# Kernel tuning notes

Measured on AMD Instinct MI355X. Metric: run time of the kernel, lower is better.

## Reference

```python
import jax, jax.numpy as jnp
import numpy as np

N_NEURON = 1024
N_PEPTIDE = 16
N_GENES = 1
BATCH = 2048
SQ = 32  # int(sqrt(N_NEURON))
DT = 1.0 / 120.0
STATE_SIZE = N_NEURON + N_GENES + N_NEURON + N_NEURON * N_PEPTIDE  # 18433


def setup_inputs() -> dict:
    key = jax.random.key(0)
    ks = jax.random.split(key, 10)
    # structured state: [ablate_mat | pc2 | neuron | peptide]
    ablate_mat = jnp.ones((BATCH, N_NEURON), jnp.float32)
    pc2 = jax.random.uniform(ks[0], (BATCH, N_GENES), jnp.float32)
    neuron = jax.random.normal(ks[1], (BATCH, N_NEURON), jnp.float32)
    peptide = jax.random.uniform(ks[2], (BATCH, N_NEURON * N_PEPTIDE), jnp.float32)
    state = jnp.concatenate([ablate_mat, pc2, neuron, peptide], axis=-1)
    u = jax.random.normal(ks[3], (BATCH, 1), jnp.float32)
    # uniform noise sample used by the exp firing noise; keep strictly < 1
    noise_u = jax.random.uniform(ks[4], (BATCH, N_NEURON), jnp.float32, 1e-6, 1.0 - 1e-6)
    D = jax.random.uniform(ks[5], (N_PEPTIDE,), jnp.float32)
    pep_prod_rate = jax.random.uniform(ks[6], (N_PEPTIDE,), jnp.float32)
    pep_decay_rate = jax.random.uniform(ks[7], (N_PEPTIDE,), jnp.float32)
    pep_action = jax.random.normal(ks[8], (N_PEPTIDE,), jnp.float32)
    synapse_matrix = jax.random.normal(ks[9], (N_NEURON, N_NEURON), jnp.float32) * 0.02
    neuron_decay = jnp.ones((1,), jnp.float32) * 0.5
    input_layer = jax.random.normal(jax.random.fold_in(key, 11), (N_NEURON,), jnp.float32)
    return dict(u=u, state=state, noise_u=noise_u, D=D, pep_prod_rate=pep_prod_rate,
                pep_decay_rate=pep_decay_rate, pep_action=pep_action,
                synapse_matrix=synapse_matrix, neuron_decay=neuron_decay,
                input_layer=input_layer)


def reference(u, state, noise_u, D, pep_prod_rate, pep_decay_rate, pep_action,
              synapse_matrix, neuron_decay, input_layer):
    # func = abs (log_train=False)
    Dp = jnp.abs(D)
    prod_r = jnp.abs(pep_prod_rate)
    decay_r = jnp.abs(pep_decay_rate)
    ndecay = jnp.abs(neuron_decay)

    # unpack state: [ablate | pc2 | neuron | peptide]
    ablate_mat = state[:, :N_NEURON]
    pc2 = state[:, N_NEURON:N_NEURON + N_GENES]
    neuron = state[:, N_NEURON + N_GENES:2 * N_NEURON + N_GENES]
    pep_flat = state[:, 2 * N_NEURON + N_GENES:]
    peptide = pep_flat.reshape(-1, N_NEURON, N_PEPTIDE)

    firing = jax.nn.relu(neuron) * ablate_mat
    neuron = neuron * ablate_mat

    # noisy_fire, noise='exp': firing = -(firing+0.01)*log(1-U)
    firing = -(firing + 0.01) * jnp.log1p(-noise_u)
    firing = jnp.clip(firing, 0.0, 10.0)

    # peptide production / decay
    pep_prod = prod_r * firing[:, :, None]           # (b, n, p)
    pep_decay = decay_r * peptide                    # (b, n, p)

    # wrap-around 2D Laplacian diffusion stencil on (SQ, SQ) grid
    ps = peptide.reshape(-1, SQ, SQ, N_PEPTIDE)
    lap = (jnp.roll(ps, -1, axis=1) + jnp.roll(ps, 1, axis=1)
           + jnp.roll(ps, -1, axis=2) + jnp.roll(ps, 1, axis=2) - 4.0 * ps)
    pep_diffuse = (Dp * lap).reshape(-1, N_NEURON, N_PEPTIDE)

    # neuron dynamics
    d_neuron = jnp.sum(peptide * pep_action, axis=-1) * pc2
    d_neuron = d_neuron + firing @ synapse_matrix
    d_neuron = d_neuron - neuron * ndecay
    d_neuron = d_neuron + input_layer * u            # (b,1)*(n,) broadcast

    d_peptide = (pep_prod - pep_decay + pep_diffuse).reshape(-1, N_NEURON * N_PEPTIDE)
    pep_new = pep_flat + d_peptide * DT
    neuron_new = (neuron + d_neuron * DT) * ablate_mat

    state_new = jnp.concatenate([ablate_mat, pc2, neuron_new, pep_new], axis=-1)
    # return_firing=True
    return firing, state_new
```

## Files before the change

kernel.cpp:

```cpp
#include <hip/hip_runtime.h>
#include <hip/hip_bf16.h>

#define N_NEURON 1024
#define N_PEPTIDE 16
#define N_GENES 1
#define BATCH 2048
#define SQ 32
#define DT_STEP (1.0f/120.0f)
#define S_STRIDE (N_NEURON + N_GENES + N_NEURON + N_NEURON*N_PEPTIDE)

typedef __attribute__((ext_vector_type(8))) short short8;
typedef __attribute__((ext_vector_type(4))) float floatx4;

__global__ __launch_bounds__(256) void synT_cast(const float* __restrict__ syn,
                                                 __hip_bfloat16* __restrict__ synT) {
    __shared__ float tile[32][33];
    const int n0 = blockIdx.x * 32;
    const int k0 = blockIdx.y * 32;
    const int tx = threadIdx.x & 31;
    const int ty = threadIdx.x >> 5;
    #pragma unroll
    for (int i = 0; i < 4; ++i)
        tile[ty + i*8][tx] = syn[(long)(k0 + ty + i*8) * N_NEURON + n0 + tx];
    __syncthreads();
    #pragma unroll
    for (int i = 0; i < 4; ++i)
        synT[(long)(n0 + ty + i*8) * N_NEURON + k0 + tx] =
            __float2bfloat16(tile[tx][ty + i*8]);
}

__global__ __launch_bounds__(256) void fused_elem(
    const float* __restrict__ u,
    const float* __restrict__ state,
    const float* __restrict__ noise,
    const float* __restrict__ D,
    const float* __restrict__ prod_g,
    const float* __restrict__ decay_g,
    const float* __restrict__ pact_g,
    const float* __restrict__ ndecay_g,
    const float* __restrict__ inL,
    float* __restrict__ firing_out,
    float* __restrict__ state_new,
    __hip_bfloat16* __restrict__ fbf)
{
    __shared__ float sf[N_NEURON];
    __shared__ float sn[N_NEURON];
    const int b = blockIdx.x;
    const int tid = threadIdx.x;
    const long bS = (long)b * S_STRIDE;
    const float u_b = u[b];
    const float pc2 = state[bS + N_NEURON];
    const float ndecay = fabsf(ndecay_g[0]);

    #pragma unroll
    for (int k = 0; k < 4; ++k) {
        const int n = tid + k * 256;
        const float ab = state[bS + n];
        const float nr = state[bS + N_NEURON + N_GENES + n];
        const float nm = nr * ab;
        float f = fmaxf(nr, 0.f) * ab;
        f = -(f + 0.01f) * log1pf(-noise[(long)b * N_NEURON + n]);
        f = fminf(fmaxf(f, 0.f), 10.f);
        firing_out[(long)b * N_NEURON + n] = f;
        fbf[(long)b * N_NEURON + n] = __float2bfloat16(f);
        state_new[bS + n] = ab;
        sf[n] = f;
        sn[n] = nm;
    }
    if (tid == 0) state_new[bS + N_NEURON] = pc2;
    __syncthreads();

    const int p = tid & 15;
    const float Dp      = fabsf(D[p]);
    const float prod_r  = fabsf(prod_g[p]);
    const float decay_r = fabsf(decay_g[p]);
    const float pact    = pact_g[p];
    const int g16 = tid >> 4;

    const float* __restrict__ pep = state + bS + 2 * N_NEURON + N_GENES;
    float* __restrict__ pep_new = state_new + bS + 2 * N_NEURON + N_GENES;

    for (int it = 0; it < 64; ++it) {
        const int n = it * 16 + g16;
        const int si = n >> 5, sj = n & 31;
        const int iup = ((((si + 31) & 31) * 32 + sj) << 4) + p;
        const int idn = ((((si + 1) & 31) * 32 + sj) << 4) + p;
        const int ilf = ((si * 32 + ((sj + 31) & 31)) << 4) + p;
        const int irt = ((si * 32 + ((sj + 1) & 31)) << 4) + p;
        const int idx = (n << 4) + p;
        const float c = pep[idx];
        const float lap = pep[iup] + pep[idn] + pep[ilf] + pep[irt] - 4.f * c;
        const float f = sf[n];
        pep_new[idx] = c + DT_STEP * (prod_r * f - decay_r * c + Dp * lap);

        float ps = c * pact;
        ps += __shfl_xor(ps, 1);
        ps += __shfl_xor(ps, 2);
        ps += __shfl_xor(ps, 4);
        ps += __shfl_xor(ps, 8);
        if (p == 0) {
            const float nm = sn[n];
            const float c0 = nm + DT_STEP * (ps * pc2 - nm * ndecay + inL[n] * u_b);
            state_new[bS + N_NEURON + N_GENES + n] = c0;
        }
    }
}

__global__ __launch_bounds__(256) void gemm_epi(
    const __hip_bfloat16* __restrict__ A,
    const __hip_bfloat16* __restrict__ BT,
    const float* __restrict__ state,
    float* __restrict__ state_new)
{
    const int tid = threadIdx.x;
    const int w = tid >> 6, lid = tid & 63;
    const int q = lid >> 4, l16 = lid & 15;
    const int m0 = blockIdx.x * 64 + (w & 1) * 32;
    const int n0 = blockIdx.y * 64 + (w >> 1) * 32;

    floatx4 acc[2][2] = {};
    for (int k0 = 0; k0 < 1024; k0 += 32) {
        short8 a[2], bfr[2];
        #pragma unroll
        for (int mi = 0; mi < 2; ++mi)
            a[mi] = *(const short8*)(A + (long)(m0 + mi * 16 + l16) * 1024 + k0 + q * 8);
        #pragma unroll
        for (int ni = 0; ni < 2; ++ni)
            bfr[ni] = *(const short8*)(BT + (long)(n0 + ni * 16 + l16) * 1024 + k0 + q * 8);
        #pragma unroll
        for (int mi = 0; mi < 2; ++mi)
            #pragma unroll
            for (int ni = 0; ni < 2; ++ni)
                acc[mi][ni] = __builtin_amdgcn_mfma_f32_16x16x32_bf16(
                    a[mi], bfr[ni], acc[mi][ni], 0, 0, 0);
    }

    #pragma unroll
    for (int mi = 0; mi < 2; ++mi)
    #pragma unroll
    for (int ni = 0; ni < 2; ++ni)
    #pragma unroll
    for (int r = 0; r < 4; ++r) {
        const int m = m0 + mi * 16 + q * 4 + r;
        const int n = n0 + ni * 16 + l16;
        const long sidx = (long)m * S_STRIDE;
        const float ab = state[sidx + n];
        const float c0 = state_new[sidx + N_NEURON + N_GENES + n];
        state_new[sidx + N_NEURON + N_GENES + n] = (c0 + DT_STEP * acc[mi][ni][r]) * ab;
    }
}

extern "C" void kernel_launch(void* const* d_in, const int* in_sizes, int n_in,
                              void* d_out, int out_size, void* d_ws, size_t ws_size,
                              hipStream_t stream) {
    const float* u      = (const float*)d_in[0];
    const float* state  = (const float*)d_in[1];
    const float* noise  = (const float*)d_in[2];
    const float* D      = (const float*)d_in[3];
    const float* prod   = (const float*)d_in[4];
    const float* decay  = (const float*)d_in[5];
    const float* pact   = (const float*)d_in[6];
    const float* syn    = (const float*)d_in[7];
    const float* ndec   = (const float*)d_in[8];
    const float* inL    = (const float*)d_in[9];

    float* firing = (float*)d_out;
    float* state_new = firing + (long)BATCH * N_NEURON;

    __hip_bfloat16* fbf  = (__hip_bfloat16*)d_ws;
    __hip_bfloat16* synT = fbf + (long)BATCH * N_NEURON;

    hipLaunchKernelGGL(synT_cast, dim3(32, 32), dim3(256), 0, stream, syn, synT);
    hipLaunchKernelGGL(fused_elem, dim3(BATCH), dim3(256), 0, stream,
                       u, state, noise, D, prod, decay, pact, ndec, inL,
                       firing, state_new, fbf);
    hipLaunchKernelGGL(gemm_epi, dim3(32, 16), dim3(256), 0, stream,
                       fbf, synT, state, state_new);
}
```

Baseline: 384.5 us.

## Vectorize elementwise/stencil kernel and stage GEMM tiles through swizzled double-buffered LDS

The elementwise kernel now processes four neurons or four peptides per thread with float4 loads and stores, and defers the neuron update to a final vectorized pass that reads peptide sums from shared memory. The GEMM stages A and B tiles into double-buffered, XOR-swizzled LDS using global_load_lds, so operands are shared across the block's waves instead of each wave reading them from global memory. Because the state stride is odd, the float4 accesses are unaligned, which may cost memory throughput. The extra barrier and LDS traffic add some synchronization overhead.

```diff
diff --git a/kernel.cpp b/kernel.cpp
--- a/kernel.cpp
+++ b/kernel.cpp
@@ -10,7 +10,9 @@
 #define S_STRIDE (N_NEURON + N_GENES + N_NEURON + N_NEURON*N_PEPTIDE)
 
 typedef __attribute__((ext_vector_type(8))) short short8;
+typedef __attribute__((ext_vector_type(4))) short short4v;
 typedef __attribute__((ext_vector_type(4))) float floatx4;
+typedef floatx4 floatx4u __attribute__((aligned(4)));
 
 __global__ __launch_bounds__(256) void synT_cast(const float* __restrict__ syn,
                                                  __hip_bfloat16* __restrict__ synT) {
@@ -45,6 +47,7 @@
 {
     __shared__ float sf[N_NEURON];
     __shared__ float sn[N_NEURON];
+    __shared__ float sps[N_NEURON];
     const int b = blockIdx.x;
     const int tid = threadIdx.x;
     const long bS = (long)b * S_STRIDE;
@@ -52,58 +55,107 @@
     const float pc2 = state[bS + N_NEURON];
     const float ndecay = fabsf(ndecay_g[0]);
 
-    #pragma unroll
-    for (int k = 0; k < 4; ++k) {
-        const int n = tid + k * 256;
-        const float ab = state[bS + n];
-        const float nr = state[bS + N_NEURON + N_GENES + n];
-        const float nm = nr * ab;
-        float f = fmaxf(nr, 0.f) * ab;
-        f = -(f + 0.01f) * log1pf(-noise[(long)b * N_NEURON + n]);
-        f = fminf(fmaxf(f, 0.f), 10.f);
-        firing_out[(long)b * N_NEURON + n] = f;
-        fbf[(long)b * N_NEURON + n] = __float2bfloat16(f);
-        state_new[bS + n] = ab;
-        sf[n] = f;
-        sn[n] = nm;
+    {
+        const int n4 = tid * 4;
+        floatx4 ab = *(const floatx4u*)(state + bS + n4);
+        floatx4 nr = *(const floatx4u*)(state + bS + N_NEURON + N_GENES + n4);
+        floatx4 nz = *(const floatx4*)(noise + (long)b * N_NEURON + n4);
+        floatx4 f, nm;
+        short4v hb;
+        #pragma unroll
+        for (int j = 0; j < 4; ++j) {
+            nm[j] = nr[j] * ab[j];
+            float fr = fmaxf(nr[j], 0.f) * ab[j];
+            fr = -(fr + 0.01f) * log1pf(-nz[j]);
+            fr = fminf(fmaxf(fr, 0.f), 10.f);
+            f[j] = fr;
+            __hip_bfloat16 h = __float2bfloat16(fr);
+            hb[j] = *reinterpret_cast<short*>(&h);
+        }
+        *(floatx4*)(firing_out + (long)b * N_NEURON + n4) = f;
+        *(short4v*)(fbf + (long)b * N_NEURON + n4) = hb;
+        *(floatx4u*)(state_new + bS + n4) = ab;
+        *(floatx4*)(sf + n4) = f;
+        *(floatx4*)(sn + n4) = nm;
     }
     if (tid == 0) state_new[bS + N_NEURON] = pc2;
     __syncthreads();
 
-    const int p = tid & 15;
-    const float Dp      = fabsf(D[p]);
-    const float prod_r  = fabsf(prod_g[p]);
-    const float decay_r = fabsf(decay_g[p]);
-    const float pact    = pact_g[p];
-    const int g16 = tid >> 4;
-
+    const int pq = tid & 3;
+    const int nl = tid >> 2;
+    const int p0 = pq * 4;
+    floatx4 Dq, prq, deq, paq;
+    #pragma unroll
+    for (int j = 0; j < 4; ++j) {
+        Dq[j]  = fabsf(D[p0 + j]);
+        prq[j] = fabsf(prod_g[p0 + j]);
+        deq[j] = fabsf(decay_g[p0 + j]);
+        paq[j] = pact_g[p0 + j];
+    }
     const float* __restrict__ pep = state + bS + 2 * N_NEURON + N_GENES;
     float* __restrict__ pep_new = state_new + bS + 2 * N_NEURON + N_GENES;
 
-    for (int it = 0; it < 64; ++it) {
-        const int n = it * 16 + g16;
+    #pragma unroll 2
+    for (int it = 0; it < 16; ++it) {
+        const int n = it * 64 + nl;
         const int si = n >> 5, sj = n & 31;
-        const int iup = ((((si + 31) & 31) * 32 + sj) << 4) + p;
-        const int idn = ((((si + 1) & 31) * 32 + sj) << 4) + p;
-        const int ilf = ((si * 32 + ((sj + 31) & 31)) << 4) + p;
-        const int irt = ((si * 32 + ((sj + 1) & 31)) << 4) + p;
-        const int idx = (n << 4) + p;
-        const float c = pep[idx];
-        const float lap = pep[iup] + pep[idn] + pep[ilf] + pep[irt] - 4.f * c;
-        const float f = sf[n];
-        pep_new[idx] = c + DT_STEP * (prod_r * f - decay_r * c + Dp * lap);
-
-        float ps = c * pact;
+        const int iup = ((((si + 31) & 31) * 32 + sj) << 4) + p0;
+        const int idn = ((((si + 1) & 31) * 32 + sj) << 4) + p0;
+        const int ilf = ((si * 32 + ((sj + 31) & 31)) << 4) + p0;
+        const int irt = ((si * 32 + ((sj + 1) & 31)) << 4) + p0;
+        const int idx = (n << 4) + p0;
+        floatx4 c  = *(const floatx4u*)(pep + idx);
+        floatx4 vu = *(const floatx4u*)(pep + iup);
+        floatx4 vd = *(const floatx4u*)(pep + idn);
+        floatx4 vl = *(const floatx4u*)(pep + ilf);
+        floatx4 vr = *(const floatx4u*)(pep + irt);
+        const float fn = sf[n];
+        floatx4 lap = vu + vd + vl + vr - 4.f * c;
+        floatx4 outv = c + DT_STEP * (prq * fn - deq * c + Dq * lap);
+        *(floatx4u*)(pep_new + idx) = outv;
+
+        float ps = c[0]*paq[0] + c[1]*paq[1] + c[2]*paq[2] + c[3]*paq[3];
         ps += __shfl_xor(ps, 1);
         ps += __shfl_xor(ps, 2);
-        ps += __shfl_xor(ps, 4);
-        ps += __shfl_xor(ps, 8);
-        if (p == 0) {
-            const float nm = sn[n];
-            const float c0 = nm + DT_STEP * (ps * pc2 - nm * ndecay + inL[n] * u_b);
-            state_new[bS + N_NEURON + N_GENES + n] = c0;
-        }
-    }
+        if (pq == 0) sps[n] = ps;
+    }
+    __syncthreads();
+
+    {
+        const int n4 = tid * 4;
+        floatx4 ss = *(const floatx4*)(sps + n4);
+        floatx4 nm = *(const floatx4*)(sn + n4);
+        floatx4 il = *(const floatx4*)(inL + n4);
+        floatx4 c0;
+        #pragma unroll
+        for (int j = 0; j < 4; ++j)
+            c0[j] = nm[j] + DT_STEP * (ss[j] * pc2 - nm[j] * ndecay + il[j] * u_b);
+        *(floatx4u*)(state_new + bS + N_NEURON + N_GENES + n4) = c0;
+    }
+}
+
+__device__ __forceinline__ void stage8k(const __hip_bfloat16* __restrict__ gbase,
+                                        char* lhalf, int row0, int k0,
+                                        int w, int lane)
+{
+    #pragma unroll
+    for (int i = 0; i < 2; ++i) {
+        const int ch  = w * 2 + i;
+        const int o   = ch * 1024 + lane * 16;
+        const int row = o >> 7;
+        const int c16 = (o >> 4) & 7;
+        const int cl  = c16 ^ (row & 7);
+        const __hip_bfloat16* g = gbase + (long)(row0 + row) * 1024 + k0 + cl * 8;
+        __builtin_amdgcn_global_load_lds(
+            (const __attribute__((address_space(1))) void*)g,
+            (__attribute__((address_space(3))) void*)(lhalf + ch * 1024),
+            16, 0, 0);
+    }
+}
+
+__device__ __forceinline__ short8 lds_frag(const char* lhalf, int row, int c16) {
+    const int cl = c16 ^ (row & 7);
+    return *(const short8*)(lhalf + row * 128 + cl * 16);
 }
 
 __global__ __launch_bounds__(256) void gemm_epi(
@@ -112,27 +164,42 @@
     const float* __restrict__ state,
     float* __restrict__ state_new)
 {
+    __shared__ __align__(16) char lds[2][16384];
     const int tid = threadIdx.x;
-    const int w = tid >> 6, lid = tid & 63;
-    const int q = lid >> 4, l16 = lid & 15;
-    const int m0 = blockIdx.x * 64 + (w & 1) * 32;
-    const int n0 = blockIdx.y * 64 + (w >> 1) * 32;
+    const int w = tid >> 6, lane = tid & 63;
+    const int q = lane >> 4, l16 = lane & 15;
+    const int m0 = blockIdx.x * 64;
+    const int n0 = blockIdx.y * 64;
+    const int wm = (w & 1) * 32, wn = (w >> 1) * 32;
 
     floatx4 acc[2][2] = {};
-    for (int k0 = 0; k0 < 1024; k0 += 32) {
-        short8 a[2], bfr[2];
+
+    stage8k(A,  lds[0],        m0, 0, w, lane);
+    stage8k(BT, lds[0] + 8192, n0, 0, w, lane);
+    __syncthreads();
+
+    int cur = 0;
+    for (int t = 0; t < 16; ++t) {
+        if (t < 15) {
+            stage8k(A,  lds[cur ^ 1],        m0, (t + 1) * 64, w, lane);
+            stage8k(BT, lds[cur ^ 1] + 8192, n0, (t + 1) * 64, w, lane);
+        }
+        const char* la = lds[cur];
+        const char* lb = lds[cur] + 8192;
         #pragma unroll
-        for (int mi = 0; mi < 2; ++mi)
-            a[mi] = *(const short8*)(A + (long)(m0 + mi * 16 + l16) * 1024 + k0 + q * 8);
-        #pragma unroll
-        for (int ni = 0; ni < 2; ++ni)
-            bfr[ni] = *(const short8*)(BT + (long)(n0 + ni * 16 + l16) * 1024 + k0 + q * 8);
-        #pragma unroll
-        for (int mi = 0; mi < 2; ++mi)
-            #pragma unroll
-            for (int ni = 0; ni < 2; ++ni)
-                acc[mi][ni] = __builtin_amdgcn_mfma_f32_16x16x32_bf16(
-                    a[mi], bfr[ni], acc[mi][ni], 0, 0, 0);
+        for (int kk = 0; kk < 2; ++kk) {
+            const int c16 = kk * 4 + q;
+            short8 a0 = lds_frag(la, wm + l16,      c16);
+            short8 a1 = lds_frag(la, wm + 16 + l16, c16);
+            short8 b0 = lds_frag(lb, wn + l16,      c16);
+            short8 b1 = lds_frag(lb, wn + 16 + l16, c16);
+            acc[0][0] = __builtin_amdgcn_mfma_f32_16x16x32_bf16(a0, b0, acc[0][0], 0, 0, 0);
+            acc[0][1] = __builtin_amdgcn_mfma_f32_16x16x32_bf16(a0, b1, acc[0][1], 0, 0, 0);
+            acc[1][0] = __builtin_amdgcn_mfma_f32_16x16x32_bf16(a1, b0, acc[1][0], 0, 0, 0);
+            acc[1][1] = __builtin_amdgcn_mfma_f32_16x16x32_bf16(a1, b1, acc[1][1], 0, 0, 0);
+        }
+        if (t < 15) __syncthreads();
+        cur ^= 1;
     }
 
     #pragma unroll
@@ -141,8 +208,8 @@
     for (int ni = 0; ni < 2; ++ni)
     #pragma unroll
     for (int r = 0; r < 4; ++r) {
-        const int m = m0 + mi * 16 + q * 4 + r;
-        const int n = n0 + ni * 16 + l16;
+        const int m = m0 + wm + mi * 16 + q * 4 + r;
+        const int n = n0 + wn + ni * 16 + l16;
         const long sidx = (long)m * S_STRIDE;
         const float ab = state[sidx + n];
         const float c0 = state_new[sidx + N_NEURON + N_GENES + n];
```

New measurement: 338.0 us. -12.1%, faster.
